# Optimization experiments

Hardware: AMD Instinct MI355X
Metric: run time of the kernel (lower is better)

## Reference

```python
import jax, jax.numpy as jnp
import numpy as np

STEP_SIZE = 0.01  # init kwarg step_size

def _quad_grad(A, b, x):
    # grad of per-node quadratic: 2*A_n @ x_n + b_n ; shapes [N,D,D],[N,D],[N,D]
    return 2.0 * jnp.einsum('nij,nj->ni', A, x) + b

def setup_inputs() -> dict:
    key = jax.random.key(0)
    kA, kb, kx, ke = jax.random.split(key, 4)
    N, D, E = 20000, 64, 320000
    A = jax.random.normal(kA, (N, D, D), dtype=jnp.float32)
    b = jax.random.normal(kb, (N, D), dtype=jnp.float32)
    x = jax.random.normal(kx, (N, D), dtype=jnp.float32)
    edge_index = jax.random.randint(ke, (2, E), 0, N, dtype=jnp.int64)
    return {"A": A, "b": b, "x": x, "edge_index": edge_index, "num_layers": 10}

def reference(A, b, x, edge_index, num_layers):
    N, D = x.shape
    src, dst = edge_index[0], edge_index[1]
    # push-sum column-stochastic mixing weights: 1/out_degree incl. self-loop
    deg = jnp.ones((N,), x.dtype).at[src].add(1.0)
    inv_deg = (1.0 / deg)[:, None]  # [N,1]

    def mix(z):  # z: [N,F]
        msg = z[src] * inv_deg[src]  # gather + weight
        agg = jax.ops.segment_sum(msg, dst, num_segments=N)
        return agg + z * inv_deg  # self-loop term

    y = _quad_grad(A, b, x)
    u = x
    v = jnp.ones((N, 1), x.dtype)
    x0 = x
    x1 = x0
    for _ in range(num_layers):
        u = mix(u - STEP_SIZE * y)          # conv on u
        v = mix(v)                           # conv on v (push-sum weight)
        x1 = u * (1.0 / v)                   # inv_v * u
        g1 = _quad_grad(A, b, x1)
        g0 = _quad_grad(A, b, x0)
        y = mix(y) + g1 - g0                 # conv on y + gradient tracking
        x0 = x1
    comm_cost = jnp.asarray(3 * num_layers * src.shape[0], dtype=jnp.int64)
    return x1, comm_cost
```

## Files before the change

kernel.cpp:

```cpp
#include <hip/hip_runtime.h>
#include <hip/hip_bf16.h>
#include <hip/hip_fp16.h>

#define STEP 0.01f
#define D 64
#define NUM_LAYERS 10

union H8 { uint4 u; __half h[8]; };

__device__ inline void add4(float4& a, const float4 b) {
    a.x += b.x; a.y += b.y; a.z += b.z; a.w += b.w;
}


__global__ void k_setup(float* __restrict__ degf, int* __restrict__ degd, int N) {
    int n = blockIdx.x * blockDim.x + threadIdx.x;
    if (n < N) { degf[n] = 1.0f; degd[n] = 0; }
}

__global__ void k_deg2(const int* __restrict__ ei, float* __restrict__ degf,
                       int* __restrict__ degd, int E) {
    int e = blockIdx.x * blockDim.x + threadIdx.x;
    if (e < E) {
        unsafeAtomicAdd(&degf[ei[e]], 1.0f);
        atomicAdd(&degd[ei[E + e]], 1);
    }
}

__global__ __launch_bounds__(1024) void k_scan(
        const int* __restrict__ degd, const float* __restrict__ degf,
        int* __restrict__ row_ptr, int* __restrict__ cursor,
        float* __restrict__ invdeg, int N, int E) {
    __shared__ int part[1024];
    int tid = threadIdx.x;
    int chunk = (N + 1023) / 1024;
    int lo = tid * chunk, hi = min(lo + chunk, N);
    int s = 0;
    for (int i = lo; i < hi; ++i) s += degd[i];
    part[tid] = s;
    __syncthreads();
    for (int off = 1; off < 1024; off <<= 1) {
        int v = (tid >= off) ? part[tid - off] : 0;
        __syncthreads();
        part[tid] += v;
        __syncthreads();
    }
    int base = (tid == 0) ? 0 : part[tid - 1];
    for (int i = lo; i < hi; ++i) {
        row_ptr[i] = base;
        cursor[i] = base;
        base += degd[i];
        invdeg[i] = 1.0f / degf[i];
    }
    if (tid == 1023) row_ptr[N] = E;
}

__global__ void k_scatter(const int* __restrict__ ei, int* __restrict__ cursor,
                          int* __restrict__ col, int E) {
    int e = blockIdx.x * blockDim.x + threadIdx.x;
    if (e < E) {
        int pos = atomicAdd(&cursor[ei[E + e]], 1);
        col[pos] = ei[e];
    }
}


__global__ __launch_bounds__(256) void k_init(
        const float* __restrict__ A, const float* __restrict__ b,
        const float* __restrict__ x, const float* __restrict__ invdeg,
        __half* __restrict__ Ah, float* __restrict__ uw, float* __restrict__ yw,
        float* __restrict__ vw, float* __restrict__ x0, int N) {
    __shared__ __align__(16) float sx[D];
    __shared__ float sy[D];
    int n = blockIdx.x, t = threadIdx.x;
    if (t < D) sx[t] = x[(size_t)n * D + t];
    __syncthreads();
    const float4* Af = (const float4*)(A + (size_t)n * D * D);
    int r = t >> 2, q = t & 3;
    float p = 0.0f;
    H8 pk0, pk1;
#pragma unroll
    for (int k = 0; k < 4; ++k) {
        float4 a = Af[t * 4 + k];
        int c = q * 16 + k * 4;
        p += a.x * sx[c] + a.y * sx[c + 1] + a.z * sx[c + 2] + a.w * sx[c + 3];
        __half* dh = ((k < 2) ? pk0.h : pk1.h) + (k & 1) * 4;
        dh[0] = __float2half(a.x);
        dh[1] = __float2half(a.y);
        dh[2] = __float2half(a.z);
        dh[3] = __float2half(a.w);
    }
    uint4* Aho = (uint4*)(Ah + (size_t)n * D * D);
    Aho[t * 2 + 0] = pk0.u;
    Aho[t * 2 + 1] = pk1.u;
    p += __shfl_xor(p, 1);
    p += __shfl_xor(p, 2);
    if (q == 0) sy[r] = 2.0f * p + b[(size_t)n * D + r];
    __syncthreads();
    if (t < D) {
        size_t off = (size_t)n * D + t;
        float wd = invdeg[n];
        float xv = sx[t];
        float yv = sy[t];
        uw[off] = (xv - STEP * yv) * wd;
        yw[off] = yv * wd;
        x0[off] = xv;
        if (t == 0) vw[n] = wd;
    }
}


__global__ __launch_bounds__(256) void k_layer(
        const __half* __restrict__ Ah,
        const int* __restrict__ row_ptr, const int* __restrict__ col,
        const float* __restrict__ uw, const float* __restrict__ yw,
        const float* __restrict__ vw, const float* __restrict__ invdeg,
        float* __restrict__ uwn, float* __restrict__ ywn, float* __restrict__ vwn,
        float* __restrict__ x0, int N) {
    __shared__ __align__(16) float su[4][D];
    __shared__ __align__(16) float sy[4][D];
    __shared__ float sv[4];
    __shared__ __align__(16) float sdx[D];
    __shared__ float sun[D];
    __shared__ float sytot[D];
    __shared__ float syn[D];
    __shared__ float svn;

    int n = blockIdx.x, t = threadIdx.x;
    int lane = t & 63, w = t >> 6;
    int j = lane >> 4, q4 = lane & 15;

    int rs = row_ptr[n], re = row_ptr[n + 1];
    float4 au = {0.f, 0.f, 0.f, 0.f}, ay = {0.f, 0.f, 0.f, 0.f};
    float av = 0.0f;
    for (int base = rs + w * 4; base < re; base += 16) {
        int e = base + j;
        if (e < re) {
            int s = col[e];
            float4 uu = ((const float4*)(uw + (size_t)s * D))[q4];
            float4 yy = ((const float4*)(yw + (size_t)s * D))[q4];
            add4(au, uu);
            add4(ay, yy);
            if (q4 == 0) av += vw[s];
        }
    }
    au.x += __shfl_xor(au.x, 16); au.y += __shfl_xor(au.y, 16);
    au.z += __shfl_xor(au.z, 16); au.w += __shfl_xor(au.w, 16);
    au.x += __shfl_xor(au.x, 32); au.y += __shfl_xor(au.y, 32);
    au.z += __shfl_xor(au.z, 32); au.w += __shfl_xor(au.w, 32);
    ay.x += __shfl_xor(ay.x, 16); ay.y += __shfl_xor(ay.y, 16);
    ay.z += __shfl_xor(ay.z, 16); ay.w += __shfl_xor(ay.w, 16);
    ay.x += __shfl_xor(ay.x, 32); ay.y += __shfl_xor(ay.y, 32);
    ay.z += __shfl_xor(ay.z, 32); ay.w += __shfl_xor(ay.w, 32);
    av += __shfl_xor(av, 16);
    av += __shfl_xor(av, 32);
    if (j == 0) {
        ((float4*)su[w])[q4] = au;
        ((float4*)sy[w])[q4] = ay;
        if (q4 == 0) sv[w] = av;
    }
    __syncthreads();

    if (w == 0) {
        size_t off = (size_t)n * D + lane;
        float ut = su[0][lane] + su[1][lane] + su[2][lane] + su[3][lane] + uw[off];
        float yt = sy[0][lane] + sy[1][lane] + sy[2][lane] + sy[3][lane] + yw[off];
        float vt = sv[0] + sv[1] + sv[2] + sv[3] + vw[n];
        float x1 = ut / vt;
        sdx[lane] = x1 - x0[off];
        x0[off] = x1;
        sun[lane] = ut;
        sytot[lane] = yt;
        if (lane == 0) svn = vt;
    }
    __syncthreads();

    {
        const uint4* Ahp = (const uint4*)(Ah + (size_t)n * D * D);
        int r = t >> 2, q = t & 3;
        float p = 0.0f;
#pragma unroll
        for (int k = 0; k < 2; ++k) {
            H8 a;
            a.u = Ahp[t * 2 + k];
            int c = q * 16 + k * 8;
#pragma unroll
            for (int jj = 0; jj < 8; ++jj)
                p += __half2float(a.h[jj]) * sdx[c + jj];
        }
        p += __shfl_xor(p, 1);
        p += __shfl_xor(p, 2);
        if (q == 0) syn[r] = sytot[r] + 2.0f * p;
    }
    __syncthreads();

    if (t < D) {
        float wd = invdeg[n];
        float ynf = syn[t];
        size_t off = (size_t)n * D + t;
        uwn[off] = (sun[t] - STEP * ynf) * wd;
        ywn[off] = ynf * wd;
        if (t == 0) vwn[n] = svn * wd;
    }
}

__global__ void k_final(const float* __restrict__ x0, float* __restrict__ out,
                        int ND, int last_idx, float comm) {
    int i = blockIdx.x * blockDim.x + threadIdx.x;
    if (i < ND) out[i] = x0[i];
    if (i == 0) out[last_idx] = comm;
}


extern "C" void kernel_launch(void* const* d_in, const int* in_sizes, int n_in,
                              void* d_out, int out_size, void* d_ws, size_t ws_size,
                              hipStream_t stream) {
    const float* A  = (const float*)d_in[0];
    const float* b  = (const float*)d_in[1];
    const float* x  = (const float*)d_in[2];
    const int*   ei = (const int*)d_in[3];

    const int N = in_sizes[1] / D;
    const int E = in_sizes[3] / 2;
    const size_t ND = (size_t)N * D;

    char* ws = (char*)d_ws;
    __half* Ah = (__half*)ws;
    float* x0   = (float*)(ws + ND * D * sizeof(__half));
    float* uw0  = x0 + ND;
    float* yw0  = uw0 + ND;
    float* uw1  = yw0 + ND;
    float* yw1  = uw1 + ND;
    float* vw0  = yw1 + ND;
    float* vw1  = vw0 + N;
    float* invdeg = vw1 + N;
    float* degf = invdeg + N;
    int* degd    = (int*)(degf + N);
    int* row_ptr = degd + N;
    int* cursor  = row_ptr + N + 4;
    int* col     = cursor + N;

    k_setup<<<(N + 255) / 256, 256, 0, stream>>>(degf, degd, N);
    k_deg2<<<(E + 255) / 256, 256, 0, stream>>>(ei, degf, degd, E);
    k_scan<<<1, 1024, 0, stream>>>(degd, degf, row_ptr, cursor, invdeg, N, E);
    k_scatter<<<(E + 255) / 256, 256, 0, stream>>>(ei, cursor, col, E);
    k_init<<<N, 256, 0, stream>>>(A, b, x, invdeg, Ah, uw0, yw0, vw0, x0, N);

    float *uc = uw0, *un = uw1, *yc = yw0, *yn = yw1, *vc = vw0, *vn = vw1;
    for (int l = 0; l < NUM_LAYERS; ++l) {
        k_layer<<<N, 256, 0, stream>>>(Ah, row_ptr, col, uc, yc, vc, invdeg,
                                       un, yn, vn, x0, N);
        float* t;
        t = uc; uc = un; un = t;
        t = yc; yc = yn; yn = t;
        t = vc; vc = vn; vn = t;
    }

    float comm = (float)(3 * NUM_LAYERS * E);
    k_final<<<((int)ND + 255) / 256, 256, 0, stream>>>(x0, (float*)d_out, (int)ND,
                                                       out_size - 1, comm);
}
```

Measured before the change: 1.045 ms.

## Pack u and y messages into interleaved half2 buffer and fuse final copy

Stores the weighted u and y node messages as one interleaved half2 array instead of two fp32 arrays. This halves the bytes moved by the random gather in each layer, at the cost of fp16 rounding on the propagated state. The final output write is folded into the last layer kernel, removing the separate copy kernel. The matvec thread mapping in k_init and k_layer is also changed to coalesced row-major access.

```diff
diff --git a/kernel.cpp b/kernel.cpp
--- a/kernel.cpp
+++ b/kernel.cpp
@@ -6,11 +6,8 @@
 #define D 64
 #define NUM_LAYERS 10
 
-union H8 { uint4 u; __half h[8]; };
-
-__device__ inline void add4(float4& a, const float4 b) {
-    a.x += b.x; a.y += b.y; a.z += b.z; a.w += b.w;
-}
+union H4 { uint2 u; __half h[4]; };
+union H8 { uint4 u; __half2 h2[4]; __half h[8]; };
 
 
 __global__ void k_setup(float* __restrict__ degf, int* __restrict__ degd, int N) {
@@ -68,43 +65,42 @@
 __global__ __launch_bounds__(256) void k_init(
         const float* __restrict__ A, const float* __restrict__ b,
         const float* __restrict__ x, const float* __restrict__ invdeg,
-        __half* __restrict__ Ah, float* __restrict__ uw, float* __restrict__ yw,
+        __half* __restrict__ Ah, __half2* __restrict__ msg,
         float* __restrict__ vw, float* __restrict__ x0, int N) {
     __shared__ __align__(16) float sx[D];
-    __shared__ float sy[D];
+    __shared__ float syv[D];
     int n = blockIdx.x, t = threadIdx.x;
+    int lane = t & 63, w = t >> 6, colgrp = lane & 15;
     if (t < D) sx[t] = x[(size_t)n * D + t];
     __syncthreads();
-    const float4* Af = (const float4*)(A + (size_t)n * D * D);
-    int r = t >> 2, q = t & 3;
-    float p = 0.0f;
-    H8 pk0, pk1;
+    const float* An = A + (size_t)n * D * D;
+    __half* Ahn = Ah + (size_t)n * D * D;
+    float4 xr = ((const float4*)sx)[colgrp];
+    int rbase = w * 16 + (lane >> 4);
 #pragma unroll
-    for (int k = 0; k < 4; ++k) {
-        float4 a = Af[t * 4 + k];
-        int c = q * 16 + k * 4;
-        p += a.x * sx[c] + a.y * sx[c + 1] + a.z * sx[c + 2] + a.w * sx[c + 3];
-        __half* dh = ((k < 2) ? pk0.h : pk1.h) + (k & 1) * 4;
-        dh[0] = __float2half(a.x);
-        dh[1] = __float2half(a.y);
-        dh[2] = __float2half(a.z);
-        dh[3] = __float2half(a.w);
-    }
-    uint4* Aho = (uint4*)(Ah + (size_t)n * D * D);
-    Aho[t * 2 + 0] = pk0.u;
-    Aho[t * 2 + 1] = pk1.u;
-    p += __shfl_xor(p, 1);
-    p += __shfl_xor(p, 2);
-    if (q == 0) sy[r] = 2.0f * p + b[(size_t)n * D + r];
+    for (int g = 0; g < 4; ++g) {
+        int row = rbase + g * 4;
+        float4 a = ((const float4*)(An + (size_t)row * D))[colgrp];
+        H4 pk;
+        pk.h[0] = __float2half(a.x);
+        pk.h[1] = __float2half(a.y);
+        pk.h[2] = __float2half(a.z);
+        pk.h[3] = __float2half(a.w);
+        ((uint2*)(Ahn + (size_t)row * D))[colgrp] = pk.u;
+        float p = a.x * xr.x + a.y * xr.y + a.z * xr.z + a.w * xr.w;
+        p += __shfl_xor(p, 1);
+        p += __shfl_xor(p, 2);
+        p += __shfl_xor(p, 4);
+        p += __shfl_xor(p, 8);
+        if (colgrp == 0) syv[row] = 2.0f * p + b[(size_t)n * D + row];
+    }
     __syncthreads();
     if (t < D) {
-        size_t off = (size_t)n * D + t;
         float wd = invdeg[n];
         float xv = sx[t];
-        float yv = sy[t];
-        uw[off] = (xv - STEP * yv) * wd;
-        yw[off] = yv * wd;
-        x0[off] = xv;
+        float yv = syv[t];
+        msg[(size_t)n * D + t] = __floats2half2_rn((xv - STEP * yv) * wd, yv * wd);
+        x0[(size_t)n * D + t] = xv;
         if (t == 0) vw[n] = wd;
     }
 }
@@ -113,12 +109,13 @@
 __global__ __launch_bounds__(256) void k_layer(
         const __half* __restrict__ Ah,
         const int* __restrict__ row_ptr, const int* __restrict__ col,
-        const float* __restrict__ uw, const float* __restrict__ yw,
-        const float* __restrict__ vw, const float* __restrict__ invdeg,
-        float* __restrict__ uwn, float* __restrict__ ywn, float* __restrict__ vwn,
-        float* __restrict__ x0, int N) {
-    __shared__ __align__(16) float su[4][D];
-    __shared__ __align__(16) float sy[4][D];
+        const __half2* __restrict__ msg, const float* __restrict__ vw,
+        const float* __restrict__ invdeg,
+        __half2* __restrict__ msgn, float* __restrict__ vwn,
+        float* __restrict__ x0, float* __restrict__ xout,
+        int last_idx, float comm, int N) {
+    __shared__ float su[4][D];
+    __shared__ float sy[4][D];
     __shared__ float sv[4];
     __shared__ __align__(16) float sdx[D];
     __shared__ float sun[D];
@@ -137,10 +134,16 @@
         int e = base + j;
         if (e < re) {
             int s = col[e];
-            float4 uu = ((const float4*)(uw + (size_t)s * D))[q4];
-            float4 yy = ((const float4*)(yw + (size_t)s * D))[q4];
-            add4(au, uu);
-            add4(ay, yy);
+            H8 m;
+            m.u = ((const uint4*)(msg + (size_t)s * D))[q4];
+            float2 f0 = __half22float2(m.h2[0]);
+            float2 f1 = __half22float2(m.h2[1]);
+            float2 f2 = __half22float2(m.h2[2]);
+            float2 f3 = __half22float2(m.h2[3]);
+            au.x += f0.x; ay.x += f0.y;
+            au.y += f1.x; ay.y += f1.y;
+            au.z += f2.x; ay.z += f2.y;
+            au.w += f3.x; ay.w += f3.y;
             if (q4 == 0) av += vw[s];
         }
     }
@@ -163,12 +166,14 @@
 
     if (w == 0) {
         size_t off = (size_t)n * D + lane;
-        float ut = su[0][lane] + su[1][lane] + su[2][lane] + su[3][lane] + uw[off];
-        float yt = sy[0][lane] + sy[1][lane] + sy[2][lane] + sy[3][lane] + yw[off];
+        float2 self = __half22float2(msg[off]);
+        float ut = su[0][lane] + su[1][lane] + su[2][lane] + su[3][lane] + self.x;
+        float yt = sy[0][lane] + sy[1][lane] + sy[2][lane] + sy[3][lane] + self.y;
         float vt = sv[0] + sv[1] + sv[2] + sv[3] + vw[n];
         float x1 = ut / vt;
         sdx[lane] = x1 - x0[off];
         x0[off] = x1;
+        if (xout) xout[off] = x1;
         sun[lane] = ut;
         sytot[lane] = yt;
         if (lane == 0) svn = vt;
@@ -177,38 +182,35 @@
 
     {
         const uint4* Ahp = (const uint4*)(Ah + (size_t)n * D * D);
-        int r = t >> 2, q = t & 3;
-        float p = 0.0f;
+        int cb = (t & 7) * 8;
+        int r0 = t >> 3;
+        H8 a0, a1;
+        a0.u = Ahp[t];
+        a1.u = Ahp[256 + t];
+        float p0 = 0.0f, p1 = 0.0f;
 #pragma unroll
-        for (int k = 0; k < 2; ++k) {
-            H8 a;
-            a.u = Ahp[t * 2 + k];
-            int c = q * 16 + k * 8;
-#pragma unroll
-            for (int jj = 0; jj < 8; ++jj)
-                p += __half2float(a.h[jj]) * sdx[c + jj];
+        for (int jj = 0; jj < 8; ++jj) {
+            float dv = sdx[cb + jj];
+            p0 += __half2float(a0.h[jj]) * dv;
+            p1 += __half2float(a1.h[jj]) * dv;
         }
-        p += __shfl_xor(p, 1);
-        p += __shfl_xor(p, 2);
-        if (q == 0) syn[r] = sytot[r] + 2.0f * p;
+        p0 += __shfl_xor(p0, 1); p1 += __shfl_xor(p1, 1);
+        p0 += __shfl_xor(p0, 2); p1 += __shfl_xor(p1, 2);
+        p0 += __shfl_xor(p0, 4); p1 += __shfl_xor(p1, 4);
+        if ((lane & 7) == 0) {
+            syn[r0]      = sytot[r0]      + 2.0f * p0;
+            syn[32 + r0] = sytot[32 + r0] + 2.0f * p1;
+        }
     }
     __syncthreads();
 
     if (t < D) {
         float wd = invdeg[n];
         float ynf = syn[t];
-        size_t off = (size_t)n * D + t;
-        uwn[off] = (sun[t] - STEP * ynf) * wd;
-        ywn[off] = ynf * wd;
+        msgn[(size_t)n * D + t] = __floats2half2_rn((sun[t] - STEP * ynf) * wd, ynf * wd);
         if (t == 0) vwn[n] = svn * wd;
     }
-}
-
-__global__ void k_final(const float* __restrict__ x0, float* __restrict__ out,
-                        int ND, int last_idx, float comm) {
-    int i = blockIdx.x * blockDim.x + threadIdx.x;
-    if (i < ND) out[i] = x0[i];
-    if (i == 0) out[last_idx] = comm;
+    if (xout && n == 0 && t == 0) xout[last_idx] = comm;
 }
 
 
@@ -226,12 +228,10 @@
 
     char* ws = (char*)d_ws;
     __half* Ah = (__half*)ws;
-    float* x0   = (float*)(ws + ND * D * sizeof(__half));
-    float* uw0  = x0 + ND;
-    float* yw0  = uw0 + ND;
-    float* uw1  = yw0 + ND;
-    float* yw1  = uw1 + ND;
-    float* vw0  = yw1 + ND;
+    __half2* msg0 = (__half2*)(ws + ND * D * sizeof(__half));
+    __half2* msg1 = msg0 + ND;
+    float* x0   = (float*)(msg1 + ND);
+    float* vw0  = x0 + ND;
     float* vw1  = vw0 + N;
     float* invdeg = vw1 + N;
     float* degf = invdeg + N;
@@ -244,19 +244,16 @@
     k_deg2<<<(E + 255) / 256, 256, 0, stream>>>(ei, degf, degd, E);
     k_scan<<<1, 1024, 0, stream>>>(degd, degf, row_ptr, cursor, invdeg, N, E);
     k_scatter<<<(E + 255) / 256, 256, 0, stream>>>(ei, cursor, col, E);
-    k_init<<<N, 256, 0, stream>>>(A, b, x, invdeg, Ah, uw0, yw0, vw0, x0, N);
-
-    float *uc = uw0, *un = uw1, *yc = yw0, *yn = yw1, *vc = vw0, *vn = vw1;
+    k_init<<<N, 256, 0, stream>>>(A, b, x, invdeg, Ah, msg0, vw0, x0, N);
+
+    float comm = (float)(3 * NUM_LAYERS * E);
+    __half2 *mc = msg0, *mn = msg1;
+    float *vc = vw0, *vn = vw1;
     for (int l = 0; l < NUM_LAYERS; ++l) {
-        k_layer<<<N, 256, 0, stream>>>(Ah, row_ptr, col, uc, yc, vc, invdeg,
-                                       un, yn, vn, x0, N);
-        float* t;
-        t = uc; uc = un; un = t;
-        t = yc; yc = yn; yn = t;
-        t = vc; vc = vn; vn = t;
-    }
-
-    float comm = (float)(3 * NUM_LAYERS * E);
-    k_final<<<((int)ND + 255) / 256, 256, 0, stream>>>(x0, (float*)d_out, (int)ND,
-                                                       out_size - 1, comm);
-}
+        float* xout = (l == NUM_LAYERS - 1) ? (float*)d_out : nullptr;
+        k_layer<<<N, 256, 0, stream>>>(Ah, row_ptr, col, mc, vc, invdeg,
+                                       mn, vn, x0, xout, out_size - 1, comm, N);
+        __half2* tm = mc; mc = mn; mn = tm;
+        float* tv = vc; vc = vn; vn = tv;
+    }
+}
```

New measurement: 964.3 us. 1.08x faster.
